# Optimization experiments

Hardware: AMD Instinct MI355X
Metric: run time of the kernel (lower is better)

## Reference

```python
import jax, jax.numpy as jnp
import numpy as np

B, L, C_IN, HID = 32, 2048, 256, 512


def setup_inputs() -> dict:
    key = jax.random.key(0)
    k1, k2, k3, k4, k5, k6 = jax.random.split(key, 6)
    x = jax.random.normal(k1, (B, L, C_IN), dtype=jnp.float32)
    y = jax.random.normal(k2, (B, L, C_IN), dtype=jnp.float32)
    # Conv1d kernel_size=1 weights, stored as [out, in] (squeezed kernel dim)
    s1 = 1.0 / np.sqrt(C_IN)
    s2 = 1.0 / np.sqrt(HID)
    W1 = jax.random.uniform(k3, (HID, C_IN), jnp.float32, -s1, s1)
    b1 = jax.random.uniform(k4, (HID,), jnp.float32, -s1, s1)
    W2 = jax.random.uniform(k5, (HID, HID), jnp.float32, -s2, s2)
    b2 = jax.random.uniform(k6, (HID,), jnp.float32, -s2, s2)
    return {"x": x, "y": y, "W1": W1, "b1": b1, "W2": W2, "b2": b2}


def _project(t, W1, b1, W2, b2):
    # t: [B, L, C_in] -> (transpose + two 1x1 convs) -> [B, HID, L]
    h = jnp.einsum('hc,blc->bhl', W1, t) + b1[None, :, None]
    h = jnp.einsum('gh,bhl->bgl', W2, h) + b2[None, :, None]
    return h


def reference(x, y, W1, b1, W2, b2):
    xp = _project(x, W1, b1, W2, b2)  # [B, HID, L]
    yp = _project(y, W1, b1, W2, b2)  # [B, HID, L]
    # grouped conv1d with groups=B*M and full-length kernel == per-channel dot product
    out = jnp.sum(jnp.tanh(xp) * jnp.tanh(yp), axis=-1)  # [B, HID]
    return out
```

## Files before the change

### kernel.cpp

```cpp
#include <hip/hip_runtime.h>
#include <hip/hip_bf16.h>

#define B_   32
#define L_   2048
#define CIN  256
#define HID  512
#define TL   16
#define TPT  16
#define NGRP 256
#define NBLK (NGRP * 4)

#define TANH_SCALE 2.885390081777927

typedef __bf16 bf16_t;
typedef __bf16 bf16x8 __attribute__((ext_vector_type(8)));
typedef __bf16 bf16x4 __attribute__((ext_vector_type(4)));
typedef float  f32x4  __attribute__((ext_vector_type(4)));

#define APIPE  8192u
#define ABUF   16384u
#define TY_OFF 32768u

__global__ void compose_kernel(const float* __restrict__ W1, const float* __restrict__ W2,
                               const float* __restrict__ b1, const float* __restrict__ b2,
                               bf16_t* __restrict__ Wc, float* __restrict__ bc)
{
    const int g = blockIdx.x;
    const int c = threadIdx.x;
    const float* w2row = W2 + (size_t)g * HID;
    float s[8] = {0.f, 0.f, 0.f, 0.f, 0.f, 0.f, 0.f, 0.f};
#pragma unroll 2
    for (int h = 0; h < HID; h += 8) {
#pragma unroll
        for (int k = 0; k < 8; ++k)
            s[k] = fmaf(w2row[h + k], W1[(size_t)(h + k) * CIN + c], s[k]);
    }
    float tot = ((s[0] + s[1]) + (s[2] + s[3])) + ((s[4] + s[5]) + (s[6] + s[7]));
    Wc[(size_t)g * CIN + c] = (bf16_t)(tot * (float)TANH_SCALE);
    if (c < 64) {
        float t = 0.f;
        for (int h = c; h < HID; h += 64)
            t = fmaf(w2row[h], b1[h], t);
#pragma unroll
        for (int off = 32; off >= 1; off >>= 1)
            t += __shfl_xor(t, off);
        if (c == 0) bc[g] = (t + b2[g]) * (float)TANH_SCALE;
    }
}

__global__ __launch_bounds__(512, 4)
void fused_kernel(const float* __restrict__ x, const float* __restrict__ y,
                  const bf16_t* __restrict__ Wc, const float* __restrict__ bc,
                  float* __restrict__ out)
{
    __shared__ char U[49152];

    const int tid  = threadIdx.x;
    const int lane = tid & 63;
    const int wv   = tid >> 6;
    const int l15  = lane & 15;
    const int l4   = lane >> 4;

    const int d    = blockIdx.x;
    const int grp  = (d & 7) + 8 * (d >> 5);
    const int q    = (d >> 3) & 3;

    const int pipe = wv >> 2;
    const int wq   = wv & 3;
    const int gc0  = q * 128 + wq * 32;

    bf16x8 wreg[8][2];
#pragma unroll
    for (int kk = 0; kk < 8; ++kk)
#pragma unroll
        for (int cj = 0; cj < 2; ++cj)
            wreg[kk][cj] = *reinterpret_cast<const bf16x8*>(
                Wc + (size_t)(gc0 + cj * 16 + l15) * CIN + kk * 32 + l4 * 8);

    f32x4 bcv[2];
#pragma unroll
    for (int cj = 0; cj < 2; ++cj) {
        float4 t4 = *reinterpret_cast<const float4*>(bc + gc0 + cj * 16 + l4 * 4);
        bcv[cj] = (f32x4){t4.x, t4.y, t4.z, t4.w};
    }

    const int sp = tid >> 8;
    const int t8 = tid & 255;
    const int sr = t8 >> 4;
    const int sq = t8 & 15;
    const unsigned sswz = (unsigned)((sr & 15) << 4);
    const unsigned soff = (unsigned)(sp * APIPE + sr * 512);
    const float* sptr = (sp ? y : x) + ((size_t)grp * (TPT * TL) + sr) * CIN;

    float4 v[4];
    auto sload = [&](const float* rowbase) {
        const float4* s4 = reinterpret_cast<const float4*>(rowbase);
#pragma unroll
        for (int c = 0; c < 4; ++c) v[c] = s4[sq + 16 * c];
    };
    auto swrite = [&](int buf) {
        char* p = U + (unsigned)(buf * ABUF) + soff;
#pragma unroll
        for (int c = 0; c < 4; ++c) {
            const int f = sq + 16 * c;
            bf16x4 h;
            h[0] = (bf16_t)v[c].x; h[1] = (bf16_t)v[c].y;
            h[2] = (bf16_t)v[c].z; h[3] = (bf16_t)v[c].w;
            *reinterpret_cast<bf16x4*>(p + (((unsigned)(8 * f)) ^ sswz)) = h;
        }
    };

    const unsigned abase = (pipe ? APIPE : 0u) +
        (unsigned)(l15 * 512) + (((unsigned)(l4 * 16)) ^ ((unsigned)(l15 << 4)));
    const unsigned tyb = TY_OFF + (unsigned)(wq * 1536 + l15 * 48 + l4 * 8);

    f32x4 psum[2];
    psum[0] = (f32x4){0.f, 0.f, 0.f, 0.f};
    psum[1] = (f32x4){0.f, 0.f, 0.f, 0.f};

    sload(sptr);
    swrite(0);
    __syncthreads();

    for (int t = 0; t < TPT; ++t) {
        const bool pf = (t + 1 < TPT);
        const int cur = t & 1;
        if (pf) {
            sptr += TL * CIN;
            sload(sptr);
        }

        f32x4 acc0 = bcv[0], acc1 = bcv[1];
        const unsigned ab = abase + (unsigned)(cur * ABUF);
        __builtin_amdgcn_s_setprio(1);
#pragma unroll
        for (int kk = 0; kk < 8; ++kk) {
            bf16x8 a = *reinterpret_cast<const bf16x8*>(U + (ab ^ (unsigned)(kk << 6)));
            acc0 = __builtin_amdgcn_mfma_f32_16x16x32_bf16(wreg[kk][0], a, acc0, 0, 0, 0);
            acc1 = __builtin_amdgcn_mfma_f32_16x16x32_bf16(wreg[kk][1], a, acc1, 0, 0, 0);
        }
        __builtin_amdgcn_s_setprio(0);

#pragma unroll
        for (int r2 = 0; r2 < 4; ++r2) {
            acc0[r2] = fmaf(-2.0f, __builtin_amdgcn_rcpf(exp2f(acc0[r2]) + 1.0f), 1.0f);
            acc1[r2] = fmaf(-2.0f, __builtin_amdgcn_rcpf(exp2f(acc1[r2]) + 1.0f), 1.0f);
        }

        if (pipe) {
            bf16x4 t0, t1;
#pragma unroll
            for (int r2 = 0; r2 < 4; ++r2) { t0[r2] = (bf16_t)acc0[r2]; t1[r2] = (bf16_t)acc1[r2]; }
            *reinterpret_cast<bf16x4*>(U + tyb + (unsigned)(cur * 8192))        = t0;
            *reinterpret_cast<bf16x4*>(U + tyb + (unsigned)(cur * 8192) + 768u) = t1;
        }

        if (pf) swrite(cur ^ 1);

        __syncthreads();

        if (!pipe) {
            bf16x4 o0 = *reinterpret_cast<const bf16x4*>(U + tyb + (unsigned)(cur * 8192));
            bf16x4 o1 = *reinterpret_cast<const bf16x4*>(U + tyb + (unsigned)(cur * 8192) + 768u);
#pragma unroll
            for (int r2 = 0; r2 < 4; ++r2) {
                psum[0][r2] = fmaf(acc0[r2], (float)o0[r2], psum[0][r2]);
                psum[1][r2] = fmaf(acc1[r2], (float)o1[r2], psum[1][r2]);
            }
        }
    }

    if (!pipe) {
#pragma unroll
        for (int cj = 0; cj < 2; ++cj)
#pragma unroll
            for (int r2 = 0; r2 < 4; ++r2) {
                float s = psum[cj][r2];
                s += __shfl_xor(s, 1);
                s += __shfl_xor(s, 2);
                s += __shfl_xor(s, 4);
                s += __shfl_xor(s, 8);
                psum[cj][r2] = s;
            }
        if (l15 == 0) {
            const int b = grp >> 3;
            float* ob = out + (size_t)b * HID + gc0 + l4 * 4;
#pragma unroll
            for (int cj = 0; cj < 2; ++cj)
#pragma unroll
                for (int r2 = 0; r2 < 4; ++r2)
                    atomicAdd(ob + cj * 16 + r2, psum[cj][r2]);
        }
    }
}

extern "C" void kernel_launch(void* const* d_in, const int* in_sizes, int n_in,
                              void* d_out, int out_size, void* d_ws, size_t ws_size,
                              hipStream_t stream)
{
    const float* x  = (const float*)d_in[0];
    const float* y  = (const float*)d_in[1];
    const float* W1 = (const float*)d_in[2];
    const float* b1 = (const float*)d_in[3];
    const float* W2 = (const float*)d_in[4];
    const float* b2 = (const float*)d_in[5];
    float* out = (float*)d_out;

    char* ws = (char*)d_ws;
    bf16_t* Wc = (bf16_t*)ws;
    float*  bc = (float*)(ws + (256 << 10));

    hipMemsetAsync(out, 0, (size_t)out_size * sizeof(float), stream);
    hipLaunchKernelGGL(compose_kernel, dim3(HID), dim3(CIN), 0, stream, W1, W2, b1, b2, Wc, bc);
    hipLaunchKernelGGL(fused_kernel, dim3(NBLK), dim3(512), 0, stream, x, y, Wc, bc, out);
}
```

Before: 87.57 us.

## Double L-tile per iteration, stream weights from global, split input staging

Each iteration now handles 32 rows of L instead of 16, with half as many iterations, and LDS grows to 80KB. The composed weights are no longer held in registers; they are reloaded from global or cache on every k-step, which frees registers for the larger accumulator tile. Input staging is split into two halves placed around the two MFMA phases to spread out global latency. The intent is fewer barriers and better MFMA amortization, at the cost of lower occupancy (launch bounds 4 to 3 and more shared memory) and repeated weight loads.

```diff
diff --git a/kernel.cpp b/kernel.cpp
--- a/kernel.cpp
+++ b/kernel.cpp
@@ -5,8 +5,8 @@
 #define L_   2048
 #define CIN  256
 #define HID  512
-#define TL   16
-#define TPT  16
+#define TL   32
+#define TPT  8
 #define NGRP 256
 #define NBLK (NGRP * 4)
 
@@ -17,9 +17,9 @@
 typedef __bf16 bf16x4 __attribute__((ext_vector_type(4)));
 typedef float  f32x4  __attribute__((ext_vector_type(4)));
 
-#define APIPE  8192u
-#define ABUF   16384u
-#define TY_OFF 32768u
+#define APIPE  16384u
+#define ABUF   32768u
+#define TY_OFF 65536u
 
 __global__ void compose_kernel(const float* __restrict__ W1, const float* __restrict__ W2,
                                const float* __restrict__ b1, const float* __restrict__ b2,
@@ -48,12 +48,12 @@
     }
 }
 
-__global__ __launch_bounds__(512, 4)
+__global__ __launch_bounds__(512, 3)
 void fused_kernel(const float* __restrict__ x, const float* __restrict__ y,
                   const bf16_t* __restrict__ Wc, const float* __restrict__ bc,
                   float* __restrict__ out)
 {
-    __shared__ char U[49152];
+    __shared__ char U[81920];
 
     const int tid  = threadIdx.x;
     const int lane = tid & 63;
@@ -69,14 +69,6 @@
     const int wq   = wv & 3;
     const int gc0  = q * 128 + wq * 32;
 
-    bf16x8 wreg[8][2];
-#pragma unroll
-    for (int kk = 0; kk < 8; ++kk)
-#pragma unroll
-        for (int cj = 0; cj < 2; ++cj)
-            wreg[kk][cj] = *reinterpret_cast<const bf16x8*>(
-                Wc + (size_t)(gc0 + cj * 16 + l15) * CIN + kk * 32 + l4 * 8);
-
     f32x4 bcv[2];
 #pragma unroll
     for (int cj = 0; cj < 2; ++cj) {
@@ -84,25 +76,30 @@
         bcv[cj] = (f32x4){t4.x, t4.y, t4.z, t4.w};
     }
 
-    const int sp = tid >> 8;
-    const int t8 = tid & 255;
-    const int sr = t8 >> 4;
-    const int sq = t8 & 15;
-    const unsigned sswz = (unsigned)((sr & 15) << 4);
-    const unsigned soff = (unsigned)(sp * APIPE + sr * 512);
-    const float* sptr = (sp ? y : x) + ((size_t)grp * (TPT * TL) + sr) * CIN;
+    const int sp   = tid >> 8;
+    const int t8   = tid & 255;
+    const int srow = t8 >> 3;
+    const int sq   = t8 & 7;
+    const unsigned sswz = (unsigned)((srow & 15) << 4);
+    const unsigned soff = (unsigned)(sp * APIPE + srow * 512);
+    const float* sptr = (sp ? y : x) + ((size_t)grp * (TPT * TL) + srow) * CIN;
 
     float4 v[4];
-    auto sload = [&](const float* rowbase) {
+    auto loadE = [&](const float* rowbase) {
         const float4* s4 = reinterpret_cast<const float4*>(rowbase);
 #pragma unroll
-        for (int c = 0; c < 4; ++c) v[c] = s4[sq + 16 * c];
+        for (int c = 0; c < 4; ++c) v[c] = s4[sq + 8 * c];
     };
-    auto swrite = [&](int buf) {
+    auto loadL = [&](const float* rowbase) {
+        const float4* s4 = reinterpret_cast<const float4*>(rowbase);
+#pragma unroll
+        for (int c = 0; c < 4; ++c) v[c] = s4[sq + 8 * (c + 4)];
+    };
+    auto writeV = [&](int buf, int half) {
         char* p = U + (unsigned)(buf * ABUF) + soff;
 #pragma unroll
         for (int c = 0; c < 4; ++c) {
-            const int f = sq + 16 * c;
+            const int f = sq + 8 * (c + half * 4);
             bf16x4 h;
             h[0] = (bf16_t)v[c].x; h[1] = (bf16_t)v[c].y;
             h[2] = (bf16_t)v[c].z; h[3] = (bf16_t)v[c].w;
@@ -110,64 +107,116 @@
         }
     };
 
-    const unsigned abase = (pipe ? APIPE : 0u) +
-        (unsigned)(l15 * 512) + (((unsigned)(l4 * 16)) ^ ((unsigned)(l15 << 4)));
-    const unsigned tyb = TY_OFF + (unsigned)(wq * 1536 + l15 * 48 + l4 * 8);
+    unsigned abase[2];
+#pragma unroll
+    for (int ri = 0; ri < 2; ++ri)
+        abase[ri] = (pipe ? APIPE : 0u) + (unsigned)((ri * 16 + l15) * 512) +
+                    (((unsigned)(l4 * 16)) ^ ((unsigned)(l15 << 4)));
+    const unsigned tyb = TY_OFF + (unsigned)(wq * 2048 + l15 * 32 + l4 * 8);
 
     f32x4 psum[2];
     psum[0] = (f32x4){0.f, 0.f, 0.f, 0.f};
     psum[1] = (f32x4){0.f, 0.f, 0.f, 0.f};
 
-    sload(sptr);
-    swrite(0);
+    loadE(sptr); writeV(0, 0);
+    loadL(sptr); writeV(0, 1);
     __syncthreads();
 
     for (int t = 0; t < TPT; ++t) {
         const bool pf = (t + 1 < TPT);
         const int cur = t & 1;
+        const float* nptr = sptr + TL * CIN;
+        if (pf) loadE(nptr);
+
+        f32x4 acc[2][2];
+#pragma unroll
+        for (int ri = 0; ri < 2; ++ri)
+#pragma unroll
+            for (int cj = 0; cj < 2; ++cj) acc[ri][cj] = bcv[cj];
+
+        const unsigned cb = (unsigned)(cur * ABUF);
+        __builtin_amdgcn_s_setprio(1);
+#pragma unroll
+        for (int kk = 0; kk < 4; ++kk) {
+            bf16x8 w[2];
+#pragma unroll
+            for (int cj = 0; cj < 2; ++cj)
+                w[cj] = *reinterpret_cast<const bf16x8*>(
+                    Wc + (size_t)(gc0 + cj * 16 + l15) * CIN + kk * 32 + l4 * 8);
+            const unsigned kx = (unsigned)(kk << 6);
+            bf16x8 a0 = *reinterpret_cast<const bf16x8*>(U + cb + (abase[0] ^ kx));
+            bf16x8 a1 = *reinterpret_cast<const bf16x8*>(U + cb + (abase[1] ^ kx));
+#pragma unroll
+            for (int cj = 0; cj < 2; ++cj) {
+                acc[0][cj] = __builtin_amdgcn_mfma_f32_16x16x32_bf16(w[cj], a0, acc[0][cj], 0, 0, 0);
+                acc[1][cj] = __builtin_amdgcn_mfma_f32_16x16x32_bf16(w[cj], a1, acc[1][cj], 0, 0, 0);
+            }
+        }
+        __builtin_amdgcn_s_setprio(0);
+
         if (pf) {
-            sptr += TL * CIN;
-            sload(sptr);
-        }
-
-        f32x4 acc0 = bcv[0], acc1 = bcv[1];
-        const unsigned ab = abase + (unsigned)(cur * ABUF);
+            writeV(cur ^ 1, 0);
+            loadL(nptr);
+        }
+
         __builtin_amdgcn_s_setprio(1);
 #pragma unroll
-        for (int kk = 0; kk < 8; ++kk) {
-            bf16x8 a = *reinterpret_cast<const bf16x8*>(U + (ab ^ (unsigned)(kk << 6)));
-            acc0 = __builtin_amdgcn_mfma_f32_16x16x32_bf16(wreg[kk][0], a, acc0, 0, 0, 0);
-            acc1 = __builtin_amdgcn_mfma_f32_16x16x32_bf16(wreg[kk][1], a, acc1, 0, 0, 0);
+        for (int kk = 4; kk < 8; ++kk) {
+            bf16x8 w[2];
+#pragma unroll
+            for (int cj = 0; cj < 2; ++cj)
+                w[cj] = *reinterpret_cast<const bf16x8*>(
+                    Wc + (size_t)(gc0 + cj * 16 + l15) * CIN + kk * 32 + l4 * 8);
+            const unsigned kx = (unsigned)(kk << 6);
+            bf16x8 a0 = *reinterpret_cast<const bf16x8*>(U + cb + (abase[0] ^ kx));
+            bf16x8 a1 = *reinterpret_cast<const bf16x8*>(U + cb + (abase[1] ^ kx));
+#pragma unroll
+            for (int cj = 0; cj < 2; ++cj) {
+                acc[0][cj] = __builtin_amdgcn_mfma_f32_16x16x32_bf16(w[cj], a0, acc[0][cj], 0, 0, 0);
+                acc[1][cj] = __builtin_amdgcn_mfma_f32_16x16x32_bf16(w[cj], a1, acc[1][cj], 0, 0, 0);
+            }
         }
         __builtin_amdgcn_s_setprio(0);
 
 #pragma unroll
-        for (int r2 = 0; r2 < 4; ++r2) {
-            acc0[r2] = fmaf(-2.0f, __builtin_amdgcn_rcpf(exp2f(acc0[r2]) + 1.0f), 1.0f);
-            acc1[r2] = fmaf(-2.0f, __builtin_amdgcn_rcpf(exp2f(acc1[r2]) + 1.0f), 1.0f);
-        }
+        for (int ri = 0; ri < 2; ++ri)
+#pragma unroll
+            for (int cj = 0; cj < 2; ++cj)
+#pragma unroll
+                for (int r2 = 0; r2 < 4; ++r2)
+                    acc[ri][cj][r2] = fmaf(-2.0f,
+                        __builtin_amdgcn_rcpf(exp2f(acc[ri][cj][r2]) + 1.0f), 1.0f);
 
         if (pipe) {
-            bf16x4 t0, t1;
-#pragma unroll
-            for (int r2 = 0; r2 < 4; ++r2) { t0[r2] = (bf16_t)acc0[r2]; t1[r2] = (bf16_t)acc1[r2]; }
-            *reinterpret_cast<bf16x4*>(U + tyb + (unsigned)(cur * 8192))        = t0;
-            *reinterpret_cast<bf16x4*>(U + tyb + (unsigned)(cur * 8192) + 768u) = t1;
-        }
-
-        if (pf) swrite(cur ^ 1);
+#pragma unroll
+            for (int ri = 0; ri < 2; ++ri)
+#pragma unroll
+                for (int cj = 0; cj < 2; ++cj) {
+                    bf16x4 tv;
+#pragma unroll
+                    for (int r2 = 0; r2 < 4; ++r2) tv[r2] = (bf16_t)acc[ri][cj][r2];
+                    *reinterpret_cast<bf16x4*>(
+                        U + tyb + (unsigned)(cur * 8192 + ri * 1024 + cj * 512)) = tv;
+                }
+        }
+
+        if (pf) writeV(cur ^ 1, 1);
 
         __syncthreads();
 
         if (!pipe) {
-            bf16x4 o0 = *reinterpret_cast<const bf16x4*>(U + tyb + (unsigned)(cur * 8192));
-            bf16x4 o1 = *reinterpret_cast<const bf16x4*>(U + tyb + (unsigned)(cur * 8192) + 768u);
-#pragma unroll
-            for (int r2 = 0; r2 < 4; ++r2) {
-                psum[0][r2] = fmaf(acc0[r2], (float)o0[r2], psum[0][r2]);
-                psum[1][r2] = fmaf(acc1[r2], (float)o1[r2], psum[1][r2]);
-            }
-        }
+#pragma unroll
+            for (int ri = 0; ri < 2; ++ri)
+#pragma unroll
+                for (int cj = 0; cj < 2; ++cj) {
+                    bf16x4 o = *reinterpret_cast<const bf16x4*>(
+                        U + tyb + (unsigned)(cur * 8192 + ri * 1024 + cj * 512));
+#pragma unroll
+                    for (int r2 = 0; r2 < 4; ++r2)
+                        psum[cj][r2] = fmaf(acc[ri][cj][r2], (float)o[r2], psum[cj][r2]);
+                }
+        }
+        sptr = nptr;
     }
 
     if (!pipe) {
```

After: 115.0 us. 31.4% more time.
